# Kernel optimization log

Measured on AMD Instinct MI355X. Metric: run time of the kernel, lower is better.

Reference implementation:

```python
import jax, jax.numpy as jnp
import numpy as np

B, C, H, W = 8, 256, 96, 96
GH, GW = 16, 16                # proto_grid
KH, KW = H // GH, W // GW      # avg-pool kernel = stride
P = GH * GW                    # local prototypes per sample
THRESH = 0.95
NORM_EPS = 1e-4


def _safe_norm(x, axis):
    # L2-normalize with norm clamped below at NORM_EPS (matches safe_norm)
    n = jnp.sqrt(jnp.sum(x * x, axis=axis, keepdims=True))
    return x / jnp.maximum(n, NORM_EPS)


def _avg_pool(x):
    # [B, c, H, W] -> [B, c, P] non-overlapping KHxKW average pooling
    b, c = x.shape[:2]
    return x.reshape(b, c, GH, KH, GW, KW).mean(axis=(3, 5)).reshape(b, c, P)


def setup_inputs() -> dict:
    key = jax.random.key(0)
    k1, k2, k3, k4 = jax.random.split(key, 4)
    qry_fts = jax.random.normal(k1, (B, C, H, W), dtype=jnp.float32)
    sup_fts = jax.random.normal(k2, (B, C, H, W), dtype=jnp.float32)
    sup_mask = (jax.random.uniform(k3, (B, 1, H, W)) > 0.02).astype(jnp.float32)
    true_bg_mask = (jax.random.uniform(k4, (B, 1, H, W)) > 0.9).astype(jnp.float32)
    return {"qry_fts": qry_fts, "sup_fts": sup_fts,
            "sup_mask": sup_mask, "true_bg_mask": true_bg_mask}


def reference(qry_fts, sup_fts, sup_mask, true_bg_mask):
    # mode='gridconv+' path, vectorized: ragged prototype selection -> masked softmax
    local_fts = _avg_pool(sup_fts).transpose(0, 2, 1)       # [B, P, C]
    local_mask = _avg_pool(sup_mask)[:, 0, :]               # [B, P]
    local_bg = _avg_pool(true_bg_mask)[:, 0, :]             # [B, P]
    valid = (local_mask > THRESH) & (local_bg < 0.5)        # [B, P] bool

    # global masked-average prototype
    gproto = jnp.sum(sup_fts * sup_mask, axis=(-1, -2)) / (
        jnp.sum(sup_mask, axis=(-1, -2)) + 1e-5)            # [B, C]

    protos = jnp.concatenate([local_fts, gproto[:, None, :]], axis=1)  # [B, P+1, C]
    valid_all = jnp.concatenate(
        [valid, jnp.ones((B, 1), dtype=bool)], axis=1)      # global always valid

    protos_n = _safe_norm(protos, axis=2)                   # [B, P+1, C]
    qry_n = _safe_norm(qry_fts, axis=1)                     # [B, C, H, W]

    # 1x1 conv with prototype weights == batched cosine similarity
    dists = jnp.einsum('bchw,bpc->bphw', qry_n, protos_n)   # [B, P+1, H, W]

    # softmax restricted to valid prototypes (invalid get weight 0)
    logits = jnp.where(valid_all[:, :, None, None], dists, -jnp.inf)
    w = jax.nn.softmax(logits, axis=1)
    pred = jnp.sum(w * dists, axis=1, keepdims=True)        # [B, 1, H, W]
    return pred
```

## Files before the change

kernel.cpp:

```cpp
#include <hip/hip_runtime.h>

#define BB 8
#define CC 256
#define HH 96
#define WW 96
#define HWW (HH*WW)
#define NLOC 256
#define PPAD 257
#define THRESH 0.95f
#define NORM_EPS 1e-4f

typedef __attribute__((ext_vector_type(8))) short bf16x8;
typedef __attribute__((ext_vector_type(4))) float f32x4;

__global__ void k01(const float* __restrict__ sup_fts,
                    const float* __restrict__ sup_mask,
                    const float* __restrict__ true_bg,
                    float* __restrict__ protos,
                    float* __restrict__ validf,
                    float* __restrict__ masksum) {
    __shared__ float red[256];
    int blk = blockIdx.x;
    int t = threadIdx.x;
    if (blk < BB * CC) {
        int b = blk >> 8, c = blk & 255;
        int gy = t >> 4, gx = t & 15;
        const float* fb = sup_fts + ((size_t)b * CC + c) * HWW;
        const float* mb = sup_mask + (size_t)b * HWW;
        int base = gy * 6 * WW + gx * 6;
        float fs = 0.f, fm = 0.f;
        for (int r = 0; r < 6; ++r) {
            const float* rowf = fb + base + r * WW;
            const float* rowm = mb + base + r * WW;
#pragma unroll
            for (int h = 0; h < 3; ++h) {
                float2 v  = *(const float2*)(rowf + 2 * h);
                float2 mk = *(const float2*)(rowm + 2 * h);
                fs += v.x + v.y;
                fm = fmaf(v.x, mk.x, fm);
                fm = fmaf(v.y, mk.y, fm);
            }
        }
        protos[((size_t)b * PPAD + t) * CC + c] = fs * (1.f / 36.f);
        red[t] = fm;
        __syncthreads();
        for (int off = 128; off > 0; off >>= 1) {
            if (t < off) red[t] += red[t + off];
            __syncthreads();
        }
        if (t == 0) protos[((size_t)b * PPAD + 256) * CC + c] = red[0];
    } else {
        int b = blk - BB * CC;
        int gy = t >> 4, gx = t & 15;
        const float* mb = sup_mask + (size_t)b * HWW;
        const float* gb = true_bg  + (size_t)b * HWW;
        int base = gy * 6 * WW + gx * 6;
        float ms = 0.f, bs = 0.f;
        for (int r = 0; r < 6; ++r) {
            const float* rowm = mb + base + r * WW;
            const float* rowg = gb + base + r * WW;
#pragma unroll
            for (int h = 0; h < 3; ++h) {
                float2 mk = *(const float2*)(rowm + 2 * h);
                float2 bg2 = *(const float2*)(rowg + 2 * h);
                ms += mk.x + mk.y;
                bs += bg2.x + bg2.y;
            }
        }
        float mmean = ms * (1.f / 36.f);
        float bmean = bs * (1.f / 36.f);
        validf[b * PPAD + t] = (mmean > THRESH && bmean < 0.5f) ? 1.f : 0.f;
        if (t == 0) validf[b * PPAD + 256] = 1.f;
        red[t] = ms;
        __syncthreads();
        for (int off = 128; off > 0; off >>= 1) {
            if (t < off) red[t] += red[t + off];
            __syncthreads();
        }
        if (t == 0) masksum[b] = red[0];
    }
}

__global__ void k2_norm(float* __restrict__ protos,
                        const float* __restrict__ masksum,
                        unsigned short* __restrict__ Bimg) {
    int bp = blockIdx.x;
    int b = bp / PPAD;
    int p = bp - b * PPAD;
    int t = threadIdx.x;
    float v = protos[((size_t)b * PPAD + p) * CC + t];
    if (p == 256) v = v / (masksum[b] + 1e-5f);
    __shared__ float red[256];
    red[t] = v * v;
    __syncthreads();
    for (int off = 128; off > 0; off >>= 1) {
        if (t < off) red[t] += red[t + off];
        __syncthreads();
    }
    float norm = sqrtf(red[0]);
    float vn = v / fmaxf(norm, NORM_EPS);
    protos[((size_t)b * PPAD + p) * CC + t] = vn;
    if (p < NLOC) {
        unsigned int u = __float_as_uint(vn);
        unsigned short hi = (unsigned short)(u >> 16);
        float lo = vn - __uint_as_float(u & 0xffff0000u);
        unsigned int ul = __float_as_uint(lo);
        unsigned short lob = (unsigned short)((ul + 0x7fffu + ((ul >> 16) & 1u)) >> 16);
        int kc = t >> 5, j = t & 31;
        size_t base = ((size_t)(b * 8 + kc) * 2) * 8192;
        Bimg[base + (size_t)p * 32 + j] = hi;
        Bimg[base + 8192 + (size_t)p * 32 + j] = lob;
    }
}

__global__ __launch_bounds__(512, 4)
void k3_mfma(const float* __restrict__ qry,
             const unsigned short* __restrict__ Bimg,
             const float* __restrict__ protos_n,
             const float* __restrict__ validf,
             float* __restrict__ out) {
    __shared__ unsigned short Albuf[2][2][2560];
    __shared__ float nrm_l[8][64], gac_l[8][64];
    __shared__ float S_l[8][64], N_l[8][64];
    __shared__ float rn_s[64], gd_s[64];

    int bid = blockIdx.x;
    int b = bid / 144;
    int tile = bid - b * 144;
    int t = threadIdx.x;
    int lane = t & 63;
    int w = t >> 6;
    int g = lane >> 4;
    int n = lane & 15;
    int px0 = tile * 64;

    int spx = t & 63;
    int k4 = (t >> 6) * 4;

    const float* qb = qry + (size_t)b * CC * HWW;
    const float* gp = protos_n + ((size_t)b * PPAD + 256) * CC;
    const unsigned short* Bb = Bimg + (size_t)b * 8 * 2 * 8192;

    f32x4 acc[4][2];
#pragma unroll
    for (int s = 0; s < 4; ++s)
#pragma unroll
        for (int c = 0; c < 2; ++c) acc[s][c] = (f32x4){0.f, 0.f, 0.f, 0.f};

    float nrm = 0.f, gac = 0.f;
    float qs[2][4], gpv[2][4];
    bf16x8 BH[2][2], BL[2][2];

#define QLOADN(KC, QP)                                                        \
    {                                                                         \
        int c0 = (KC) * 32 + k4;                                              \
        _Pragma("unroll")                                                     \
        for (int j = 0; j < 4; ++j) {                                         \
            qs[QP][j]  = qb[(size_t)(c0 + j) * HWW + px0 + spx];              \
            gpv[QP][j] = gp[c0 + j];                                          \
        }                                                                     \
    }

#define LOADB(KC, BUF)                                                        \
    {                                                                         \
        _Pragma("unroll")                                                     \
        for (int ct = 0; ct < 2; ++ct) {                                      \
            const unsigned short* p0 = Bb + (size_t)(KC) * 16384 +            \
                                       (w * 32 + ct * 16 + n) * 32 + g * 8;   \
            BH[BUF][ct] = *(const bf16x8*)(p0);                               \
            BL[BUF][ct] = *(const bf16x8*)(p0 + 8192);                        \
        }                                                                     \
    }

#define SPLITW(QP, BUF)                                                       \
    {                                                                         \
        unsigned int hh[4], ll[4];                                            \
        _Pragma("unroll")                                                     \
        for (int j = 0; j < 4; ++j) {                                         \
            float qv = qs[QP][j];                                             \
            unsigned int u = __float_as_uint(qv);                             \
            hh[j] = u >> 16;                                                  \
            float lof = qv - __uint_as_float(u & 0xffff0000u);                \
            unsigned int ul = __float_as_uint(lof);                           \
            ll[j] = (ul + 0x7fffu + ((ul >> 16) & 1u)) >> 16;                 \
            nrm = fmaf(qv, qv, nrm);                                          \
            gac = fmaf(qv, gpv[QP][j], gac);                                  \
        }                                                                     \
        uint2 Hp, Lp;                                                         \
        Hp.x = hh[0] | (hh[1] << 16); Hp.y = hh[2] | (hh[3] << 16);           \
        Lp.x = ll[0] | (ll[1] << 16); Lp.y = ll[2] | (ll[3] << 16);           \
        *(uint2*)&Albuf[BUF][0][spx * 40 + k4] = Hp;                          \
        *(uint2*)&Albuf[BUF][1][spx * 40 + k4] = Lp;                          \
    }

    LOADB(0, 0);
    QLOADN(0, 0);
    LOADB(1, 1);
    QLOADN(1, 1);
    SPLITW(0, 0);
    __syncthreads();

#pragma unroll
    for (int kc = 0; kc < 8; ++kc) {
        if (kc < 6) QLOADN(kc + 2, kc & 1);
#pragma unroll
        for (int sub = 0; sub < 4; ++sub) {
            bf16x8 AHf = *(const bf16x8*)&Albuf[kc & 1][0][(sub * 16 + n) * 40 + g * 8];
            bf16x8 ALf = *(const bf16x8*)&Albuf[kc & 1][1][(sub * 16 + n) * 40 + g * 8];
#pragma unroll
            for (int ct = 0; ct < 2; ++ct) {
                acc[sub][ct] = __builtin_amdgcn_mfma_f32_16x16x32_bf16(AHf, BH[kc & 1][ct], acc[sub][ct], 0, 0, 0);
                acc[sub][ct] = __builtin_amdgcn_mfma_f32_16x16x32_bf16(ALf, BH[kc & 1][ct], acc[sub][ct], 0, 0, 0);
                acc[sub][ct] = __builtin_amdgcn_mfma_f32_16x16x32_bf16(AHf, BL[kc & 1][ct], acc[sub][ct], 0, 0, 0);
            }
        }
        if (kc < 6) LOADB(kc + 2, kc & 1);
        if (kc < 7) {
            SPLITW((kc + 1) & 1, (kc + 1) & 1);
            __syncthreads();
        }
    }

    nrm_l[w][spx] = nrm;
    gac_l[w][spx] = gac;
    __syncthreads();
    if (t < 64) {
        float n2 = 0.f, gs = 0.f;
#pragma unroll
        for (int i = 0; i < 8; ++i) { n2 += nrm_l[i][t]; gs += gac_l[i][t]; }
        float rn = 1.f / fmaxf(sqrtf(n2), NORM_EPS);
        rn_s[t] = rn;
        gd_s[t] = gs * rn;
    }
    __syncthreads();

    float vf0 = validf[b * PPAD + w * 32 + n];
    float vf1 = validf[b * PPAD + w * 32 + 16 + n];
#pragma unroll
    for (int sub = 0; sub < 4; ++sub) {
#pragma unroll
        for (int r = 0; r < 4; ++r) {
            int px = sub * 16 + 4 * g + r;
            float rnv = rn_s[px];
            float d0 = acc[sub][0][r] * rnv;
            float d1 = acc[sub][1][r] * rnv;
            float l0 = (vf0 != 0.f) ? d0 : -1e30f;
            float l1 = (vf1 != 0.f) ? d1 : -1e30f;
            float e0 = __expf(l0 - 1.1f);
            float e1 = __expf(l1 - 1.1f);
            float s = e0 + e1;
            float nn = fmaf(e0, l0, e1 * l1);
#pragma unroll
            for (int m = 1; m < 16; m <<= 1) {
                s  += __shfl_xor(s, m);
                nn += __shfl_xor(nn, m);
            }
            if (n == 0) { S_l[w][px] = s; N_l[w][px] = nn; }
        }
    }
    __syncthreads();

    if (t < 64) {
        float gdv = gd_s[t];
        float eg = __expf(gdv - 1.1f);
        float S = eg, N = eg * gdv;
#pragma unroll
        for (int i = 0; i < 8; ++i) { S += S_l[i][t]; N += N_l[i][t]; }
        out[(size_t)b * HWW + px0 + t] = N / S;
    }

#undef QLOADN
#undef LOADB
#undef SPLITW
}

extern "C" void kernel_launch(void* const* d_in, const int* in_sizes, int n_in,
                              void* d_out, int out_size, void* d_ws, size_t ws_size,
                              hipStream_t stream) {
    const float* qry = (const float*)d_in[0];
    const float* sup = (const float*)d_in[1];
    const float* msk = (const float*)d_in[2];
    const float* bg  = (const float*)d_in[3];
    float* out = (float*)d_out;

    float* ws = (float*)d_ws;
    float* protos  = ws;
    float* validf  = protos + (size_t)BB * PPAD * CC;
    float* masksum = validf + (size_t)BB * PPAD;
    unsigned short* Bimg = (unsigned short*)(masksum + BB);

    hipLaunchKernelGGL(k01, dim3(BB * CC + BB), dim3(256), 0, stream,
                       sup, msk, bg, protos, validf, masksum);
    hipLaunchKernelGGL(k2_norm, dim3(BB * PPAD), dim3(256), 0, stream, protos, masksum, Bimg);
    hipLaunchKernelGGL(k3_mfma, dim3(BB * (HWW / 64)), dim3(512), 0, stream,
                       qry, Bimg, protos, validf, out);
}
```

Baseline: 71.59 us.

## Restructure k3 MFMA to 16 waves with register-resident prototypes

The main GEMM kernel now runs 1024 threads per block, with each wave covering 16 prototypes instead of 32. All eight K-chunks of that wave's prototype hi/lo fragments are preloaded into registers, so the per-iteration B loads go away. Query loads become float2 per thread with a three-slot prefetch, and the operands are swapped so the softmax reduction runs mostly in registers with fewer shuffles. The trade-offs are higher register pressure under launch_bounds(1024,4) and scattered 2-byte LDS writes that may cause bank conflicts.

Result: slower. 95.52 us (+33.4%).

```diff
diff --git a/kernel.cpp b/kernel.cpp
--- a/kernel.cpp
+++ b/kernel.cpp
@@ -113,15 +113,24 @@
     }
 }
 
-__global__ __launch_bounds__(512, 4)
+#define LBAR()  do {                                             \
+        asm volatile("s_waitcnt lgkmcnt(0)" ::: "memory");       \
+        __builtin_amdgcn_sched_barrier(0);                       \
+        __builtin_amdgcn_s_barrier();                            \
+        __builtin_amdgcn_sched_barrier(0);                       \
+    } while (0)
+
+__global__ __launch_bounds__(1024, 4)
 void k3_mfma(const float* __restrict__ qry,
              const unsigned short* __restrict__ Bimg,
              const float* __restrict__ protos_n,
              const float* __restrict__ validf,
              float* __restrict__ out) {
-    __shared__ unsigned short Albuf[2][2][2560];
-    __shared__ float nrm_l[8][64], gac_l[8][64];
-    __shared__ float S_l[8][64], N_l[8][64];
+    __shared__ alignas(16) unsigned short Qlds[2][2][2560];
+    __shared__ float nrm_l[32][64];
+    __shared__ float gac_l[32][64];
+    __shared__ float S_l[16][64];
+    __shared__ float N_l[16][64];
     __shared__ float rn_s[64], gd_s[64];
 
     int bid = blockIdx.x;
@@ -134,129 +143,112 @@
     int n = lane & 15;
     int px0 = tile * 64;
 
-    int spx = t & 63;
-    int k4 = (t >> 6) * 4;
-
-    const float* qb = qry + (size_t)b * CC * HWW;
+    int cl = t >> 5;
+    int pp = (t & 31) * 2;
+
+    const float* qb = qry + (size_t)b * CC * HWW + px0 + pp;
     const float* gp = protos_n + ((size_t)b * PPAD + 256) * CC;
     const unsigned short* Bb = Bimg + (size_t)b * 8 * 2 * 8192;
 
-    f32x4 acc[4][2];
-#pragma unroll
-    for (int s = 0; s < 4; ++s)
-#pragma unroll
-        for (int c = 0; c < 2; ++c) acc[s][c] = (f32x4){0.f, 0.f, 0.f, 0.f};
-
-    float nrm = 0.f, gac = 0.f;
-    float qs[2][4], gpv[2][4];
-    bf16x8 BH[2][2], BL[2][2];
-
-#define QLOADN(KC, QP)                                                        \
+    bf16x8 PH[8], PL[8];
+#pragma unroll
+    for (int kc = 0; kc < 8; ++kc) {
+        const unsigned short* p0 = Bb + (size_t)kc * 16384 + (w * 16 + n) * 32 + g * 8;
+        PH[kc] = *(const bf16x8*)(p0);
+        PL[kc] = *(const bf16x8*)(p0 + 8192);
+    }
+    float gpv8[8];
+#pragma unroll
+    for (int kc = 0; kc < 8; ++kc) gpv8[kc] = gp[kc * 32 + cl];
+
+    f32x4 acc[4];
+#pragma unroll
+    for (int s = 0; s < 4; ++s) acc[s] = (f32x4){0.f, 0.f, 0.f, 0.f};
+    float nrm2[2] = {0.f, 0.f};
+    float gac2[2] = {0.f, 0.f};
+    float2 qs[3];
+
+#define QLOAD(KC, SLOT)                                                       \
+    qs[SLOT] = *(const float2*)(qb + (size_t)((KC) * 32 + cl) * HWW);
+
+#define SPLIT(KC, SLOT, BUF)                                                  \
     {                                                                         \
-        int c0 = (KC) * 32 + k4;                                              \
-        _Pragma("unroll")                                                     \
-        for (int j = 0; j < 4; ++j) {                                         \
-            qs[QP][j]  = qb[(size_t)(c0 + j) * HWW + px0 + spx];              \
-            gpv[QP][j] = gp[c0 + j];                                          \
-        }                                                                     \
-    }
-
-#define LOADB(KC, BUF)                                                        \
-    {                                                                         \
-        _Pragma("unroll")                                                     \
-        for (int ct = 0; ct < 2; ++ct) {                                      \
-            const unsigned short* p0 = Bb + (size_t)(KC) * 16384 +            \
-                                       (w * 32 + ct * 16 + n) * 32 + g * 8;   \
-            BH[BUF][ct] = *(const bf16x8*)(p0);                               \
-            BL[BUF][ct] = *(const bf16x8*)(p0 + 8192);                        \
-        }                                                                     \
-    }
-
-#define SPLITW(QP, BUF)                                                       \
-    {                                                                         \
-        unsigned int hh[4], ll[4];                                            \
-        _Pragma("unroll")                                                     \
-        for (int j = 0; j < 4; ++j) {                                         \
-            float qv = qs[QP][j];                                             \
-            unsigned int u = __float_as_uint(qv);                             \
-            hh[j] = u >> 16;                                                  \
-            float lof = qv - __uint_as_float(u & 0xffff0000u);                \
-            unsigned int ul = __float_as_uint(lof);                           \
-            ll[j] = (ul + 0x7fffu + ((ul >> 16) & 1u)) >> 16;                 \
-            nrm = fmaf(qv, qv, nrm);                                          \
-            gac = fmaf(qv, gpv[QP][j], gac);                                  \
-        }                                                                     \
-        uint2 Hp, Lp;                                                         \
-        Hp.x = hh[0] | (hh[1] << 16); Hp.y = hh[2] | (hh[3] << 16);           \
-        Lp.x = ll[0] | (ll[1] << 16); Lp.y = ll[2] | (ll[3] << 16);           \
-        *(uint2*)&Albuf[BUF][0][spx * 40 + k4] = Hp;                          \
-        *(uint2*)&Albuf[BUF][1][spx * 40 + k4] = Lp;                          \
-    }
-
-    LOADB(0, 0);
-    QLOADN(0, 0);
-    LOADB(1, 1);
-    QLOADN(1, 1);
-    SPLITW(0, 0);
-    __syncthreads();
+        float2 qv = qs[SLOT];                                                 \
+        unsigned int ux = __float_as_uint(qv.x);                              \
+        unsigned int uy = __float_as_uint(qv.y);                              \
+        unsigned short hx = (unsigned short)(ux >> 16);                       \
+        unsigned short hy = (unsigned short)(uy >> 16);                       \
+        float lxf = qv.x - __uint_as_float(ux & 0xffff0000u);                 \
+        float lyf = qv.y - __uint_as_float(uy & 0xffff0000u);                 \
+        unsigned int ulx = __float_as_uint(lxf);                              \
+        unsigned int uly = __float_as_uint(lyf);                              \
+        unsigned short lx = (unsigned short)((ulx + 0x7fffu + ((ulx >> 16) & 1u)) >> 16); \
+        unsigned short ly = (unsigned short)((uly + 0x7fffu + ((uly >> 16) & 1u)) >> 16); \
+        Qlds[BUF][0][pp * 40 + cl] = hx;                                      \
+        Qlds[BUF][0][(pp + 1) * 40 + cl] = hy;                                \
+        Qlds[BUF][1][pp * 40 + cl] = lx;                                      \
+        Qlds[BUF][1][(pp + 1) * 40 + cl] = ly;                                \
+        nrm2[0] = fmaf(qv.x, qv.x, nrm2[0]);                                  \
+        nrm2[1] = fmaf(qv.y, qv.y, nrm2[1]);                                  \
+        float gpc = gpv8[KC];                                                 \
+        gac2[0] = fmaf(qv.x, gpc, gac2[0]);                                   \
+        gac2[1] = fmaf(qv.y, gpc, gac2[1]);                                   \
+    }
+
+    QLOAD(0, 0);
+    QLOAD(1, 1);
+    QLOAD(2, 2);
+    SPLIT(0, 0, 0);
+    LBAR();
 
 #pragma unroll
     for (int kc = 0; kc < 8; ++kc) {
-        if (kc < 6) QLOADN(kc + 2, kc & 1);
+        if (kc + 3 < 8) { QLOAD(kc + 3, (kc + 3) % 3); }
 #pragma unroll
         for (int sub = 0; sub < 4; ++sub) {
-            bf16x8 AHf = *(const bf16x8*)&Albuf[kc & 1][0][(sub * 16 + n) * 40 + g * 8];
-            bf16x8 ALf = *(const bf16x8*)&Albuf[kc & 1][1][(sub * 16 + n) * 40 + g * 8];
-#pragma unroll
-            for (int ct = 0; ct < 2; ++ct) {
-                acc[sub][ct] = __builtin_amdgcn_mfma_f32_16x16x32_bf16(AHf, BH[kc & 1][ct], acc[sub][ct], 0, 0, 0);
-                acc[sub][ct] = __builtin_amdgcn_mfma_f32_16x16x32_bf16(ALf, BH[kc & 1][ct], acc[sub][ct], 0, 0, 0);
-                acc[sub][ct] = __builtin_amdgcn_mfma_f32_16x16x32_bf16(AHf, BL[kc & 1][ct], acc[sub][ct], 0, 0, 0);
-            }
-        }
-        if (kc < 6) LOADB(kc + 2, kc & 1);
-        if (kc < 7) {
-            SPLITW((kc + 1) & 1, (kc + 1) & 1);
-            __syncthreads();
-        }
-    }
-
-    nrm_l[w][spx] = nrm;
-    gac_l[w][spx] = gac;
+            bf16x8 QH = *(const bf16x8*)&Qlds[kc & 1][0][(sub * 16 + n) * 40 + g * 8];
+            bf16x8 QL = *(const bf16x8*)&Qlds[kc & 1][1][(sub * 16 + n) * 40 + g * 8];
+            acc[sub] = __builtin_amdgcn_mfma_f32_16x16x32_bf16(PH[kc], QH, acc[sub], 0, 0, 0);
+            acc[sub] = __builtin_amdgcn_mfma_f32_16x16x32_bf16(PL[kc], QH, acc[sub], 0, 0, 0);
+            acc[sub] = __builtin_amdgcn_mfma_f32_16x16x32_bf16(PH[kc], QL, acc[sub], 0, 0, 0);
+        }
+        if (kc + 1 < 8) {
+            SPLIT(kc + 1, (kc + 1) % 3, (kc + 1) & 1);
+            LBAR();
+        }
+    }
+
+    nrm_l[cl][pp] = nrm2[0]; nrm_l[cl][pp + 1] = nrm2[1];
+    gac_l[cl][pp] = gac2[0]; gac_l[cl][pp + 1] = gac2[1];
     __syncthreads();
     if (t < 64) {
         float n2 = 0.f, gs = 0.f;
 #pragma unroll
-        for (int i = 0; i < 8; ++i) { n2 += nrm_l[i][t]; gs += gac_l[i][t]; }
+        for (int i = 0; i < 32; ++i) { n2 += nrm_l[i][t]; gs += gac_l[i][t]; }
         float rn = 1.f / fmaxf(sqrtf(n2), NORM_EPS);
         rn_s[t] = rn;
         gd_s[t] = gs * rn;
     }
     __syncthreads();
 
-    float vf0 = validf[b * PPAD + w * 32 + n];
-    float vf1 = validf[b * PPAD + w * 32 + 16 + n];
+    float vfr[4];
+#pragma unroll
+    for (int r = 0; r < 4; ++r) vfr[r] = validf[b * PPAD + w * 16 + 4 * g + r];
 #pragma unroll
     for (int sub = 0; sub < 4; ++sub) {
+        float rnv = rn_s[sub * 16 + n];
+        float s = 0.f, nn = 0.f;
 #pragma unroll
         for (int r = 0; r < 4; ++r) {
-            int px = sub * 16 + 4 * g + r;
-            float rnv = rn_s[px];
-            float d0 = acc[sub][0][r] * rnv;
-            float d1 = acc[sub][1][r] * rnv;
-            float l0 = (vf0 != 0.f) ? d0 : -1e30f;
-            float l1 = (vf1 != 0.f) ? d1 : -1e30f;
-            float e0 = __expf(l0 - 1.1f);
-            float e1 = __expf(l1 - 1.1f);
-            float s = e0 + e1;
-            float nn = fmaf(e0, l0, e1 * l1);
-#pragma unroll
-            for (int m = 1; m < 16; m <<= 1) {
-                s  += __shfl_xor(s, m);
-                nn += __shfl_xor(nn, m);
-            }
-            if (n == 0) { S_l[w][px] = s; N_l[w][px] = nn; }
-        }
+            float d = acc[sub][r] * rnv;
+            float l = (vfr[r] != 0.f) ? d : -1e30f;
+            float e = __expf(l - 1.1f);
+            s += e;
+            nn = fmaf(e, l, nn);
+        }
+        s  += __shfl_xor(s, 16);  s  += __shfl_xor(s, 32);
+        nn += __shfl_xor(nn, 16); nn += __shfl_xor(nn, 32);
+        if (g == sub) { S_l[w][sub * 16 + n] = s; N_l[w][sub * 16 + n] = nn; }
     }
     __syncthreads();
 
@@ -265,13 +257,12 @@
         float eg = __expf(gdv - 1.1f);
         float S = eg, N = eg * gdv;
 #pragma unroll
-        for (int i = 0; i < 8; ++i) { S += S_l[i][t]; N += N_l[i][t]; }
+        for (int i = 0; i < 16; ++i) { S += S_l[i][t]; N += N_l[i][t]; }
         out[(size_t)b * HWW + px0 + t] = N / S;
     }
 
-#undef QLOADN
-#undef LOADB
-#undef SPLITW
+#undef QLOAD
+#undef SPLIT
 }
 
 extern "C" void kernel_launch(void* const* d_in, const int* in_sizes, int n_in,
@@ -292,6 +283,6 @@
     hipLaunchKernelGGL(k01, dim3(BB * CC + BB), dim3(256), 0, stream,
                        sup, msk, bg, protos, validf, masksum);
     hipLaunchKernelGGL(k2_norm, dim3(BB * PPAD), dim3(256), 0, stream, protos, masksum, Bimg);
-    hipLaunchKernelGGL(k3_mfma, dim3(BB * (HWW / 64)), dim3(512), 0, stream,
+    hipLaunchKernelGGL(k3_mfma, dim3(BB * (HWW / 64)), dim3(1024), 0, stream,
                        qry, Bimg, protos, validf, out);
 }
```

## Switch to fp16 split-precision MFMA with whole-tile LDS staging of query

Applied to the files above, without the earlier changes.

Replaces the bf16 hi/lo split (3 MFMAs per block) with an fp16 hi/lo split on the query and a single fp16 prototype, so only 2 MFMAs per block are issued and the prototype image is half the size. The query tile is now loaded and converted into LDS in one pass up front, using an XOR-swizzled layout, instead of being double-buffered per k-chunk. This removes the per-chunk barriers. LDS use grows to 64KB and launch bounds drop to 2 blocks per CU, which may reduce occupancy and latency hiding. Rounding the prototype to fp16 also slightly lowers accuracy.

Result: slower. 80.79 us (+12.9%).

```diff
diff --git a/kernel.cpp b/kernel.cpp
--- a/kernel.cpp
+++ b/kernel.cpp
@@ -10,8 +10,10 @@
 #define THRESH 0.95f
 #define NORM_EPS 1e-4f
 
-typedef __attribute__((ext_vector_type(8))) short bf16x8;
+typedef __attribute__((ext_vector_type(8))) _Float16 f16x8;
 typedef __attribute__((ext_vector_type(4))) float f32x4;
+
+union H16 { _Float16 f; unsigned short u; };
 
 __global__ void k01(const float* __restrict__ sup_fts,
                     const float* __restrict__ sup_mask,
@@ -83,7 +85,7 @@
 
 __global__ void k2_norm(float* __restrict__ protos,
                         const float* __restrict__ masksum,
-                        unsigned short* __restrict__ Bimg) {
+                        unsigned short* __restrict__ Pimg) {
     int bp = blockIdx.x;
     int b = bp / PPAD;
     int p = bp - b * PPAD;
@@ -101,25 +103,19 @@
     float vn = v / fmaxf(norm, NORM_EPS);
     protos[((size_t)b * PPAD + p) * CC + t] = vn;
     if (p < NLOC) {
-        unsigned int u = __float_as_uint(vn);
-        unsigned short hi = (unsigned short)(u >> 16);
-        float lo = vn - __uint_as_float(u & 0xffff0000u);
-        unsigned int ul = __float_as_uint(lo);
-        unsigned short lob = (unsigned short)((ul + 0x7fffu + ((ul >> 16) & 1u)) >> 16);
+        H16 h; h.f = (_Float16)vn;
         int kc = t >> 5, j = t & 31;
-        size_t base = ((size_t)(b * 8 + kc) * 2) * 8192;
-        Bimg[base + (size_t)p * 32 + j] = hi;
-        Bimg[base + 8192 + (size_t)p * 32 + j] = lob;
-    }
-}
-
-__global__ __launch_bounds__(512, 4)
+        Pimg[(size_t)(b * 8 + kc) * 8192 + p * 32 + j] = h.u;
+    }
+}
+
+__global__ __launch_bounds__(512, 2)
 void k3_mfma(const float* __restrict__ qry,
-             const unsigned short* __restrict__ Bimg,
+             const unsigned short* __restrict__ Pimg,
              const float* __restrict__ protos_n,
              const float* __restrict__ validf,
              float* __restrict__ out) {
-    __shared__ unsigned short Albuf[2][2][2560];
+    __shared__ alignas(16) unsigned short Qlds[64 * 512];
     __shared__ float nrm_l[8][64], gac_l[8][64];
     __shared__ float S_l[8][64], N_l[8][64];
     __shared__ float rn_s[64], gd_s[64];
@@ -133,93 +129,79 @@
     int g = lane >> 4;
     int n = lane & 15;
     int px0 = tile * 64;
-
-    int spx = t & 63;
-    int k4 = (t >> 6) * 4;
-
-    const float* qb = qry + (size_t)b * CC * HWW;
+    int spx = lane;
+
+    const float* qb = qry + (size_t)b * CC * HWW + px0 + spx;
     const float* gp = protos_n + ((size_t)b * PPAD + 256) * CC;
-    const unsigned short* Bb = Bimg + (size_t)b * 8 * 2 * 8192;
+    const unsigned short* Pb = Pimg + (size_t)b * 8 * 8192;
+
+    float nrm = 0.f, gac = 0.f;
+    int permw = ((spx & 15) << 2) | (spx >> 4);
+#pragma unroll
+    for (int j = 0; j < 8; ++j) {
+        int c0 = j * 32 + w * 4;
+        float v[4];
+#pragma unroll
+        for (int i = 0; i < 4; ++i) v[i] = qb[(size_t)(c0 + i) * HWW];
+        unsigned int hh[4], ll[4];
+#pragma unroll
+        for (int i = 0; i < 4; ++i) {
+            H16 x; x.f = (_Float16)v[i];
+            float lof = v[i] - (float)x.f;
+            H16 y; y.f = (_Float16)lof;
+            hh[i] = x.u; ll[i] = y.u;
+            nrm = fmaf(v[i], v[i], nrm);
+            gac = fmaf(v[i], gp[c0 + i], gac);
+        }
+        uint4 pk;
+        pk.x = hh[0] | (hh[1] << 16); pk.y = hh[2] | (hh[3] << 16);
+        pk.z = ll[0] | (ll[1] << 16); pk.w = ll[2] | (ll[3] << 16);
+        int kq = j * 8 + w;
+        int slot = kq ^ permw;
+        *(uint4*)&Qlds[spx * 512 + slot * 8] = pk;
+    }
+    __syncthreads();
 
     f32x4 acc[4][2];
 #pragma unroll
     for (int s = 0; s < 4; ++s)
 #pragma unroll
         for (int c = 0; c < 2; ++c) acc[s][c] = (f32x4){0.f, 0.f, 0.f, 0.f};
-
-    float nrm = 0.f, gac = 0.f;
-    float qs[2][4], gpv[2][4];
-    bf16x8 BH[2][2], BL[2][2];
-
-#define QLOADN(KC, QP)                                                        \
-    {                                                                         \
-        int c0 = (KC) * 32 + k4;                                              \
-        _Pragma("unroll")                                                     \
-        for (int j = 0; j < 4; ++j) {                                         \
-            qs[QP][j]  = qb[(size_t)(c0 + j) * HWW + px0 + spx];              \
-            gpv[QP][j] = gp[c0 + j];                                          \
-        }                                                                     \
-    }
+    f16x8 Bf[2][2];
 
 #define LOADB(KC, BUF)                                                        \
     {                                                                         \
         _Pragma("unroll")                                                     \
-        for (int ct = 0; ct < 2; ++ct) {                                      \
-            const unsigned short* p0 = Bb + (size_t)(KC) * 16384 +            \
-                                       (w * 32 + ct * 16 + n) * 32 + g * 8;   \
-            BH[BUF][ct] = *(const bf16x8*)(p0);                               \
-            BL[BUF][ct] = *(const bf16x8*)(p0 + 8192);                        \
-        }                                                                     \
-    }
-
-#define SPLITW(QP, BUF)                                                       \
-    {                                                                         \
-        unsigned int hh[4], ll[4];                                            \
-        _Pragma("unroll")                                                     \
-        for (int j = 0; j < 4; ++j) {                                         \
-            float qv = qs[QP][j];                                             \
-            unsigned int u = __float_as_uint(qv);                             \
-            hh[j] = u >> 16;                                                  \
-            float lof = qv - __uint_as_float(u & 0xffff0000u);                \
-            unsigned int ul = __float_as_uint(lof);                           \
-            ll[j] = (ul + 0x7fffu + ((ul >> 16) & 1u)) >> 16;                 \
-            nrm = fmaf(qv, qv, nrm);                                          \
-            gac = fmaf(qv, gpv[QP][j], gac);                                  \
-        }                                                                     \
-        uint2 Hp, Lp;                                                         \
-        Hp.x = hh[0] | (hh[1] << 16); Hp.y = hh[2] | (hh[3] << 16);           \
-        Lp.x = ll[0] | (ll[1] << 16); Lp.y = ll[2] | (ll[3] << 16);           \
-        *(uint2*)&Albuf[BUF][0][spx * 40 + k4] = Hp;                          \
-        *(uint2*)&Albuf[BUF][1][spx * 40 + k4] = Lp;                          \
+        for (int ct = 0; ct < 2; ++ct)                                        \
+            Bf[BUF][ct] = *(const f16x8*)(Pb + (size_t)(KC) * 8192 +          \
+                                          (w * 32 + ct * 16 + n) * 32 + g * 8); \
     }
 
     LOADB(0, 0);
-    QLOADN(0, 0);
     LOADB(1, 1);
-    QLOADN(1, 1);
-    SPLITW(0, 0);
-    __syncthreads();
 
 #pragma unroll
     for (int kc = 0; kc < 8; ++kc) {
-        if (kc < 6) QLOADN(kc + 2, kc & 1);
 #pragma unroll
         for (int sub = 0; sub < 4; ++sub) {
-            bf16x8 AHf = *(const bf16x8*)&Albuf[kc & 1][0][(sub * 16 + n) * 40 + g * 8];
-            bf16x8 ALf = *(const bf16x8*)&Albuf[kc & 1][1][(sub * 16 + n) * 40 + g * 8];
+            int row = sub * 16 + n;
+            int permr = ((row & 15) << 2) | (row >> 4);
+            int slot0 = (kc * 8 + g * 2) ^ permr;
+            const unsigned short* rp = &Qlds[row * 512];
+            uint4 Aq = *(const uint4*)&rp[slot0 * 8];
+            uint4 Bq = *(const uint4*)&rp[(slot0 ^ 1) * 8];
+            union { f16x8 v; unsigned int u[4]; } QH, QL;
+            QH.u[0] = Aq.x; QH.u[1] = Aq.y; QH.u[2] = Bq.x; QH.u[3] = Bq.y;
+            QL.u[0] = Aq.z; QL.u[1] = Aq.w; QL.u[2] = Bq.z; QL.u[3] = Bq.w;
 #pragma unroll
             for (int ct = 0; ct < 2; ++ct) {
-                acc[sub][ct] = __builtin_amdgcn_mfma_f32_16x16x32_bf16(AHf, BH[kc & 1][ct], acc[sub][ct], 0, 0, 0);
-                acc[sub][ct] = __builtin_amdgcn_mfma_f32_16x16x32_bf16(ALf, BH[kc & 1][ct], acc[sub][ct], 0, 0, 0);
-                acc[sub][ct] = __builtin_amdgcn_mfma_f32_16x16x32_bf16(AHf, BL[kc & 1][ct], acc[sub][ct], 0, 0, 0);
-            }
-        }
-        if (kc < 6) LOADB(kc + 2, kc & 1);
-        if (kc < 7) {
-            SPLITW((kc + 1) & 1, (kc + 1) & 1);
-            __syncthreads();
-        }
-    }
+                acc[sub][ct] = __builtin_amdgcn_mfma_f32_16x16x32_f16(QH.v, Bf[kc & 1][ct], acc[sub][ct], 0, 0, 0);
+                acc[sub][ct] = __builtin_amdgcn_mfma_f32_16x16x32_f16(QL.v, Bf[kc & 1][ct], acc[sub][ct], 0, 0, 0);
+            }
+        }
+        if (kc + 2 < 8) LOADB(kc + 2, kc & 1);
+    }
+#undef LOADB
 
     nrm_l[w][spx] = nrm;
     gac_l[w][spx] = gac;
@@ -268,10 +250,6 @@
         for (int i = 0; i < 8; ++i) { S += S_l[i][t]; N += N_l[i][t]; }
         out[(size_t)b * HWW + px0 + t] = N / S;
     }
-
-#undef QLOADN
-#undef LOADB
-#undef SPLITW
 }
 
 extern "C" void kernel_launch(void* const* d_in, const int* in_sizes, int n_in,
@@ -287,11 +265,11 @@
     float* protos  = ws;
     float* validf  = protos + (size_t)BB * PPAD * CC;
     float* masksum = validf + (size_t)BB * PPAD;
-    unsigned short* Bimg = (unsigned short*)(masksum + BB);
+    unsigned short* Pimg = (unsigned short*)(masksum + BB);
 
     hipLaunchKernelGGL(k01, dim3(BB * CC + BB), dim3(256), 0, stream,
                        sup, msk, bg, protos, validf, masksum);
-    hipLaunchKernelGGL(k2_norm, dim3(BB * PPAD), dim3(256), 0, stream, protos, masksum, Bimg);
+    hipLaunchKernelGGL(k2_norm, dim3(BB * PPAD), dim3(256), 0, stream, protos, masksum, Pimg);
     hipLaunchKernelGGL(k3_mfma, dim3(BB * (HWW / 64)), dim3(512), 0, stream,
-                       qry, Bimg, protos, validf, out);
-}
+                       qry, Pimg, protos, validf, out);
+}
```
